# Performance work log

Hardware: AMD Instinct MI355X
Metric: run time of the kernel (lower is better)

Reference implementation:

```python
import jax, jax.numpy as jnp
import numpy as np

D_MODEL = 1024
N_HEADS = 16
D_HEAD = D_MODEL // N_HEADS
SPARSE_THRESH = 0.09
MASK_FILL = -1e9


def setup_inputs() -> dict:
    key = jax.random.key(0)
    ks = jax.random.split(key, 11)
    B, S, D = 4, 1024, D_MODEL
    # Xavier-uniform bound for square [D, D] linear weights
    bound = float(np.sqrt(6.0 / (D + D)))

    def xavier(k):
        return jax.random.uniform(k, (D, D), jnp.float32, -bound, bound)

    return {
        "q": jax.random.normal(ks[0], (B, S, D), jnp.float32),
        "k": jax.random.normal(ks[1], (B, S, D), jnp.float32),
        "v": jax.random.normal(ks[2], (B, S, D), jnp.float32),
        "Wq": xavier(ks[3]), "bq": jnp.zeros((D,), jnp.float32),
        "Wk": xavier(ks[4]), "bk": jnp.zeros((D,), jnp.float32),
        "Wv": xavier(ks[5]), "bv": jnp.zeros((D,), jnp.float32),
        "Wo": xavier(ks[6]), "bo": jnp.zeros((D,), jnp.float32),
    }


def reference(q, k, v, Wq, bq, Wk, bk, Wv, bv, Wo, bo):
    B, S, D = q.shape
    H, dk = N_HEADS, D_HEAD

    def proj(x, W, b):
        # nn.Linear: x @ W^T + b, then split heads -> [B, H, S, dk]
        y = jnp.einsum("bsd,ed->bse", x, W) + b
        return y.reshape(B, S, H, dk).transpose(0, 2, 1, 3)

    qh = proj(q, Wq, bq)
    kh = proj(k, Wk, bk)
    vh = proj(v, Wv, bv)

    scale = 1.0 / jnp.sqrt(jnp.asarray(dk, q.dtype))
    scores = jnp.einsum("bhqd,bhkd->bhqk", qh, kh) * scale  # [B,H,S,S]

    att1 = jax.nn.softmax(scores, axis=-1)
    # mask entries whose first-pass probability is below the sparsity threshold
    scores2 = jnp.where(att1 < SPARSE_THRESH, jnp.asarray(MASK_FILL, scores.dtype), scores)
    att2 = jax.nn.softmax(scores2, axis=-1)
    # dropout(p=0.2) is identity in eval mode (deterministic reference)

    ctx = jnp.einsum("bhqk,bhkd->bhqd", att2, vh)           # [B,H,S,dk]
    ctx = ctx.transpose(0, 2, 1, 3).reshape(B, S, D)
    return jnp.einsum("bsd,ed->bse", ctx, Wo) + bo
```

## Files before the change

### kernel.cpp

```cpp
#include <hip/hip_runtime.h>
#include <hip/hip_bf16.h>
#include <math.h>


constexpr int D_MODEL = 1024;
constexpr int N_HEADS = 16;
constexpr int D_HEAD  = 64;
constexpr int SEQ     = 1024;
constexpr int BATCH   = 4;
constexpr float SPARSE_THRESH = 0.09f;

typedef short  bf16x8 __attribute__((ext_vector_type(8)));
typedef float  f32x4  __attribute__((ext_vector_type(4)));

__device__ __forceinline__ unsigned short f2bf_rne(float x) {
    unsigned u = __float_as_uint(x);
    u += 0x7FFFu + ((u >> 16) & 1u);
    return (unsigned short)(u >> 16);
}
__device__ __forceinline__ float bf2f(unsigned short b) {
    return __uint_as_float(((unsigned)b) << 16);
}

__device__ __forceinline__ unsigned cvt2(float a, float b) {
    __hip_bfloat162 p = __float22bfloat162_rn(make_float2(a, b));
    unsigned u; __builtin_memcpy(&u, &p, 4); return u;
}
__device__ __forceinline__ void split4(float x0, float x1, float x2, float x3,
                                       unsigned* hw, unsigned* lw) {
    const unsigned uh0 = cvt2(x0, x1);
    hw[0] = uh0;
    lw[0] = cvt2(x0 - __uint_as_float(uh0 << 16),
                 x1 - __uint_as_float(uh0 & 0xFFFF0000u));
    const unsigned uh1 = cvt2(x2, x3);
    hw[1] = uh1;
    lw[1] = cvt2(x2 - __uint_as_float(uh1 << 16),
                 x3 - __uint_as_float(uh1 & 0xFFFF0000u));
}

union BF8 { unsigned u[4]; bf16x8 v; };

__device__ __forceinline__ void unpack_pair(const unsigned* u, bf16x8& hi, bf16x8& lo) {
    BF8 h, l;
    #pragma unroll
    for (int p = 0; p < 4; ++p) {
        h.u[p] = (u[2 * p] >> 16)      | (u[2 * p + 1] & 0xFFFF0000u);
        l.u[p] = (u[2 * p] & 0xFFFFu)  | (u[2 * p + 1] << 16);
    }
    hi = h.v; lo = l.v;
}

__device__ __forceinline__ void gld_lds16(const void* g, void* l) {
    __builtin_amdgcn_global_load_lds(
        (const __attribute__((address_space(1))) void*)g,
        (__attribute__((address_space(3))) void*)l, 16, 0, 0);
}

__global__ __launch_bounds__(256)
void conv_w(const float* __restrict__ Wq, const float* __restrict__ Wk,
            const float* __restrict__ Wv,
            unsigned short* __restrict__ Wqh, unsigned short* __restrict__ Wql,
            unsigned short* __restrict__ Wkh, unsigned short* __restrict__ Wkl,
            unsigned short* __restrict__ Wvh, unsigned short* __restrict__ Wvl)
{
    const int NW8 = (D_MODEL * D_MODEL) / 8;
    int i = blockIdx.x * 256 + threadIdx.x;
    const float* s; unsigned short *dh, *dl;
    if (i < NW8)            { s = Wq; dh = Wqh; dl = Wql; }
    else if (i < 2 * NW8)   { i -= NW8; s = Wk; dh = Wkh; dl = Wkl; }
    else                    { i -= 2 * NW8; s = Wv; dh = Wvh; dl = Wvl; }
    const float4 x0 = ((const float4*)(s + (size_t)i * 8))[0];
    const float4 x1 = ((const float4*)(s + (size_t)i * 8))[1];
    unsigned hw[4], lw[4];
    split4(x0.x, x0.y, x0.z, x0.w, &hw[0], &lw[0]);
    split4(x1.x, x1.y, x1.z, x1.w, &hw[2], &lw[2]);
    *(uint4*)&dh[(size_t)i * 8] = *(const uint4*)hw;
    *(uint4*)&dl[(size_t)i * 8] = *(const uint4*)lw;
}

__global__ __launch_bounds__(256, 3)
void proj_qkv(const float* __restrict__ q, const float* __restrict__ k,
              const float* __restrict__ v,
              const unsigned short* __restrict__ Wqh, const unsigned short* __restrict__ Wql,
              const unsigned short* __restrict__ Wkh, const unsigned short* __restrict__ Wkl,
              const unsigned short* __restrict__ Wvh, const unsigned short* __restrict__ Wvl,
              const float* __restrict__ bq, const float* __restrict__ bk,
              const float* __restrict__ bv,
              unsigned* __restrict__ qp,
              unsigned short* __restrict__ khh, unsigned short* __restrict__ khl,
              unsigned short* __restrict__ vt)
{
    __shared__ unsigned short SM[4][128][40];
    unsigned short (*A_h)[40] = SM[0];
    unsigned short (*A_l)[40] = SM[1];
    unsigned short (*B_h)[40] = SM[2];
    unsigned short (*B_l)[40] = SM[3];

    const int z = blockIdx.z;
    const float* X    = (z == 0) ? q   : (z == 1) ? k   : v;
    const unsigned short* Wh = (z == 0) ? Wqh : (z == 1) ? Wkh : Wvh;
    const unsigned short* Wl = (z == 0) ? Wql : (z == 1) ? Wkl : Wvl;
    const float* bias = (z == 0) ? bq  : (z == 1) ? bk  : bv;

    const int K = D_MODEL;
    const int tid = threadIdx.x, lane = tid & 63;
    const int l15 = lane & 15, l4 = lane >> 4;
    const int wv4 = tid >> 6;
    const int wr = (wv4 >> 1) * 64, wc = (wv4 & 1) * 64;
    const int bm = blockIdx.x * 128, bn = blockIdx.y * 128;
    const int sr = tid >> 1, sh = (tid & 1) * 16;

    f32x4 acc[4][4];
    #pragma unroll
    for (int i = 0; i < 4; ++i)
        #pragma unroll
        for (int j = 0; j < 4; ++j) acc[i][j] = (f32x4){0.f, 0.f, 0.f, 0.f};

    const float* ga = X + (size_t)(bm + sr) * K + sh;
    const unsigned short* gbh = Wh + (size_t)(bn + sr) * K + sh;
    const unsigned short* gbl = Wl + (size_t)(bn + sr) * K + sh;

    float4 av[4];
    uint4 wbh0, wbh1, wbl0, wbl1;
    #pragma unroll
    for (int l = 0; l < 4; ++l) av[l] = *(const float4*)&ga[l * 4];
    wbh0 = *(const uint4*)&gbh[0]; wbh1 = *(const uint4*)&gbh[8];
    wbl0 = *(const uint4*)&gbl[0]; wbl1 = *(const uint4*)&gbl[8];

    #pragma unroll 1
    for (int k0 = 0; k0 < K; k0 += 32) {
        unsigned ahw[8], alw[8];
        #pragma unroll
        for (int l = 0; l < 4; ++l)
            split4(av[l].x, av[l].y, av[l].z, av[l].w, &ahw[l * 2], &alw[l * 2]);

        __syncthreads();
        *(uint4*)&A_h[sr][sh]     = *(const uint4*)&ahw[0];
        *(uint4*)&A_h[sr][sh + 8] = *(const uint4*)&ahw[4];
        *(uint4*)&A_l[sr][sh]     = *(const uint4*)&alw[0];
        *(uint4*)&A_l[sr][sh + 8] = *(const uint4*)&alw[4];
        *(uint4*)&B_h[sr][sh]     = wbh0;
        *(uint4*)&B_h[sr][sh + 8] = wbh1;
        *(uint4*)&B_l[sr][sh]     = wbl0;
        *(uint4*)&B_l[sr][sh + 8] = wbl1;
        __syncthreads();

        if (k0 + 32 < K) {
            const int o = k0 + 32;
            #pragma unroll
            for (int l = 0; l < 4; ++l) av[l] = *(const float4*)&ga[o + l * 4];
            wbh0 = *(const uint4*)&gbh[o]; wbh1 = *(const uint4*)&gbh[o + 8];
            wbl0 = *(const uint4*)&gbl[o]; wbl1 = *(const uint4*)&gbl[o + 8];
        }

        bf16x8 ah[4], al4[4], bh4[4], bl4[4];
        #pragma unroll
        for (int i = 0; i < 4; ++i) {
            const int r = wr + i * 16 + l15;
            const int c = wc + i * 16 + l15;
            ah[i]  = *(const bf16x8*)&A_h[r][l4 * 8];
            al4[i] = *(const bf16x8*)&A_l[r][l4 * 8];
            bh4[i] = *(const bf16x8*)&B_h[c][l4 * 8];
            bl4[i] = *(const bf16x8*)&B_l[c][l4 * 8];
        }
        #pragma unroll
        for (int i = 0; i < 4; ++i)
            #pragma unroll
            for (int j = 0; j < 4; ++j) {
                acc[i][j] = __builtin_amdgcn_mfma_f32_16x16x32_bf16(ah[i],  bh4[j], acc[i][j], 0, 0, 0);
                acc[i][j] = __builtin_amdgcn_mfma_f32_16x16x32_bf16(ah[i],  bl4[j], acc[i][j], 0, 0, 0);
                acc[i][j] = __builtin_amdgcn_mfma_f32_16x16x32_bf16(al4[i], bh4[j], acc[i][j], 0, 0, 0);
            }
    }

    if (z == 2) {
        unsigned short* T = &SM[0][0][0];
        __syncthreads();
        #pragma unroll
        for (int i = 0; i < 4; ++i)
            #pragma unroll
            for (int j = 0; j < 4; ++j) {
                const int cl = wc + j * 16 + l15;
                const int sl = wr + i * 16 + l4 * 4;
                const float bi = bias[bn + cl];
                unsigned short h4[4];
                #pragma unroll
                for (int r = 0; r < 4; ++r)
                    h4[r] = f2bf_rne(acc[i][j][r] + bi);
                *(uint2*)&T[cl * 136 + sl] = *(const uint2*)&h4[0];
            }
        __syncthreads();
        const int c = tid >> 1, half = tid & 1;
        const int bb = bm >> 10;
        const int sb = (bm & (SEQ - 1)) + half * 64;
        unsigned short* dst = vt + (((size_t)bb << 20) + (size_t)(bn + c) * SEQ + sb);
        const unsigned short* srcT = &T[c * 136 + half * 64];
        #pragma unroll
        for (int u = 0; u < 8; ++u)
            *(uint4*)&dst[u * 8] = *(const uint4*)&srcT[u * 8];
        return;
    }

    if (z == 0) {
        #pragma unroll
        for (int i = 0; i < 4; ++i)
            #pragma unroll
            for (int j = 0; j < 4; ++j) {
                const int rb = bm + wr + i * 16 + l4 * 4;
                const int c  = bn + wc + j * 16 + l15;
                const float bi = bias[c];
                const int h = c >> 6, d = c & (D_HEAD - 1);
                #pragma unroll
                for (int r = 0; r < 4; ++r) {
                    const float val = (acc[i][j][r] + bi) * 0.125f;
                    const unsigned short hu = f2bf_rne(val);
                    const unsigned short lu = f2bf_rne(val - bf2f(hu));
                    const int mrow = rb + r;
                    const int b = mrow >> 10, s = mrow & (SEQ - 1);
                    qp[((size_t)(b * N_HEADS + h) * SEQ + s) * D_HEAD + d] =
                        ((unsigned)hu << 16) | lu;
                }
            }
    } else {
        #pragma unroll
        for (int i = 0; i < 4; ++i)
            #pragma unroll
            for (int j = 0; j < 4; ++j) {
                const int rb = bm + wr + i * 16 + l4 * 4;
                const int c  = bn + wc + j * 16 + l15;
                const float bi = bias[c];
                const int h = c >> 6, d = c & (D_HEAD - 1);
                #pragma unroll
                for (int r = 0; r < 4; ++r) {
                    const float val = acc[i][j][r] + bi;
                    const unsigned short hu = f2bf_rne(val);
                    const unsigned short lu = f2bf_rne(val - bf2f(hu));
                    const int mrow = rb + r;
                    const int b = mrow >> 10, s = mrow & (SEQ - 1);
                    const int dsw = d ^ ((s & 7) << 3);
                    const size_t off = ((size_t)(b * N_HEADS + h) * SEQ + s) * D_HEAD + dsw;
                    khh[off] = hu;
                    khl[off] = lu;
                }
            }
    }
}

__global__ __launch_bounds__(256, 3)
void proj_o(const unsigned short* __restrict__ Act, const float* __restrict__ W,
            const float* __restrict__ bias, float* __restrict__ out)
{
    __shared__ unsigned short A_h[128][40];
    __shared__ unsigned short B_h[128][40];

    const int K = D_MODEL;
    const int tid = threadIdx.x, lane = tid & 63;
    const int l15 = lane & 15, l4 = lane >> 4;
    const int wv4 = tid >> 6;
    const int wr = (wv4 >> 1) * 64, wc = (wv4 & 1) * 64;
    const int bm = blockIdx.x * 128, bn = blockIdx.y * 128;
    const int sr = tid >> 1, sh = (tid & 1) * 16;

    f32x4 acc[4][4];
    #pragma unroll
    for (int i = 0; i < 4; ++i)
        #pragma unroll
        for (int j = 0; j < 4; ++j) acc[i][j] = (f32x4){0.f, 0.f, 0.f, 0.f};

    const unsigned short* ga = Act + (size_t)(bm + sr) * K + sh;
    const float* gb = W + (size_t)(bn + sr) * K + sh;

    uint4 av0 = *(const uint4*)&ga[0], av1 = *(const uint4*)&ga[8];
    float4 bv4[4];
    #pragma unroll
    for (int l = 0; l < 4; ++l) bv4[l] = *(const float4*)&gb[l * 4];

    #pragma unroll 1
    for (int k0 = 0; k0 < K; k0 += 32) {
        unsigned bhw[8];
        #pragma unroll
        for (int l = 0; l < 4; ++l) {
            bhw[l * 2]     = cvt2(bv4[l].x, bv4[l].y);
            bhw[l * 2 + 1] = cvt2(bv4[l].z, bv4[l].w);
        }

        __syncthreads();
        *(uint4*)&A_h[sr][sh]     = av0;
        *(uint4*)&A_h[sr][sh + 8] = av1;
        *(uint4*)&B_h[sr][sh]     = *(const uint4*)&bhw[0];
        *(uint4*)&B_h[sr][sh + 8] = *(const uint4*)&bhw[4];
        __syncthreads();

        if (k0 + 32 < K) {
            av0 = *(const uint4*)&ga[k0 + 32];
            av1 = *(const uint4*)&ga[k0 + 32 + 8];
            #pragma unroll
            for (int l = 0; l < 4; ++l)
                bv4[l] = *(const float4*)&gb[k0 + 32 + l * 4];
        }

        bf16x8 ah[4], bh4[4];
        #pragma unroll
        for (int i = 0; i < 4; ++i) {
            ah[i]  = *(const bf16x8*)&A_h[wr + i * 16 + l15][l4 * 8];
            bh4[i] = *(const bf16x8*)&B_h[wc + i * 16 + l15][l4 * 8];
        }
        #pragma unroll
        for (int i = 0; i < 4; ++i)
            #pragma unroll
            for (int j = 0; j < 4; ++j)
                acc[i][j] = __builtin_amdgcn_mfma_f32_16x16x32_bf16(ah[i], bh4[j], acc[i][j], 0, 0, 0);
    }

    #pragma unroll
    for (int i = 0; i < 4; ++i)
        #pragma unroll
        for (int j = 0; j < 4; ++j) {
            const int rb = bm + wr + i * 16 + l4 * 4;
            const int c  = bn + wc + j * 16 + l15;
            const float bi = bias[c];
            #pragma unroll
            for (int r = 0; r < 4; ++r)
                out[(size_t)(rb + r) * D_MODEL + c] = acc[i][j][r] + bi;
        }
}

__device__ __forceinline__ void score_from_lds(
    const unsigned short (* __restrict__ KH)[64], const unsigned short (* __restrict__ KL)[64],
    int l15, int dk0, int dk1,
    const bf16x8 (&qh)[2][2], const bf16x8 (&ql)[2][2], f32x4 acc[2][4])
{
    #pragma unroll
    for (int j = 0; j < 4; ++j) {
        const int row = l15 + 16 * j;
        const bf16x8 kh0 = *(const bf16x8*)&KH[row][dk0];
        const bf16x8 kh1 = *(const bf16x8*)&KH[row][dk1];
        const bf16x8 kl0 = *(const bf16x8*)&KL[row][dk0];
        const bf16x8 kl1 = *(const bf16x8*)&KL[row][dk1];
        #pragma unroll
        for (int st = 0; st < 2; ++st) {
            f32x4 a = (f32x4){0.f, 0.f, 0.f, 0.f};
            a = __builtin_amdgcn_mfma_f32_16x16x32_bf16(qh[st][0], kh0, a, 0, 0, 0);
            a = __builtin_amdgcn_mfma_f32_16x16x32_bf16(qh[st][0], kl0, a, 0, 0, 0);
            a = __builtin_amdgcn_mfma_f32_16x16x32_bf16(ql[st][0], kh0, a, 0, 0, 0);
            a = __builtin_amdgcn_mfma_f32_16x16x32_bf16(qh[st][1], kh1, a, 0, 0, 0);
            a = __builtin_amdgcn_mfma_f32_16x16x32_bf16(qh[st][1], kl1, a, 0, 0, 0);
            a = __builtin_amdgcn_mfma_f32_16x16x32_bf16(ql[st][1], kh1, a, 0, 0, 0);
            acc[st][j] = a;
        }
    }
}

__global__ __launch_bounds__(256, 3)
void attn_mfma(const unsigned* __restrict__ qp,
               const unsigned short* __restrict__ khh, const unsigned short* __restrict__ khl,
               const unsigned short* __restrict__ vt, unsigned short* __restrict__ ctxh)
{
    __shared__ unsigned short KHL[2][2][64][64];
    __shared__ unsigned short Wl[4][32][64];
    __shared__ float Vm[64];
    __shared__ int AnyNU;
    float (*Pm)[4] = (float (*)[4])&Wl[0][0][0];

    const int tid  = threadIdx.x;
    const int lane = tid & 63;
    const int wv   = tid >> 6;
    const int l15  = lane & 15, l4 = lane >> 4;
    const int bh   = blockIdx.x;
    const int b    = bh >> 4, h = bh & 15;
    const int q0   = blockIdx.y * 128 + wv * 32;

    const int swz = (l15 & 7) << 3;
    const int dk0 = (l4 * 8) ^ swz;
    const int dk1 = (32 + l4 * 8) ^ swz;

    bf16x8 qh[2][2], ql[2][2];
    #pragma unroll
    for (int st = 0; st < 2; ++st) {
        const unsigned* qrow = qp + ((size_t)bh * SEQ + q0 + st * 16 + l15) * D_HEAD;
        #pragma unroll
        for (int ks = 0; ks < 2; ++ks) {
            unsigned u[8];
            *(uint4*)&u[0] = *(const uint4*)&qrow[ks * 32 + l4 * 8];
            *(uint4*)&u[4] = *(const uint4*)&qrow[ks * 32 + l4 * 8 + 4];
            unpack_pair(u, qh[st][ks], ql[st][ks]);
        }
    }

    const unsigned short* vtb = vt + (size_t)bh * D_HEAD * SEQ;

    {
        const int d = tid >> 2, q4 = tid & 3;
        const unsigned short* vr = vtb + (size_t)d * SEQ + q4 * 256;
        float s0 = 0.f, s1 = 0.f, s2 = 0.f, s3 = 0.f;
        #pragma unroll 4
        for (int i = 0; i < 32; ++i) {
            bf16x8 v8 = *(const bf16x8*)&vr[i * 8];
            s0 += bf2f((unsigned short)v8[0]) + bf2f((unsigned short)v8[4]);
            s1 += bf2f((unsigned short)v8[1]) + bf2f((unsigned short)v8[5]);
            s2 += bf2f((unsigned short)v8[2]) + bf2f((unsigned short)v8[6]);
            s3 += bf2f((unsigned short)v8[3]) + bf2f((unsigned short)v8[7]);
        }
        Pm[d][q4] = (s0 + s1) + (s2 + s3);
        if (tid == 0) AnyNU = 0;
    }

    const size_t kbase = (size_t)bh * SEQ * D_HEAD;
    const int krow0 = wv * 16 + (lane >> 3);
    const int dgrp  = (lane & 7) * 8;

    #pragma unroll
    for (int t = 0; t < 2; ++t) {
        const size_t src = kbase + (size_t)(krow0 + t * 8) * D_HEAD + dgrp;
        gld_lds16(khh + src, &KHL[0][0][wv * 16 + t * 8][0]);
        gld_lds16(khl + src, &KHL[0][1][wv * 16 + t * 8][0]);
    }
    __syncthreads();

    if (tid < 64)
        Vm[tid] = (Pm[tid][0] + Pm[tid][1] + Pm[tid][2] + Pm[tid][3]) * (1.f / 1024.f);

    float mloc[2][4], zloc[2][4];
    #pragma unroll
    for (int st = 0; st < 2; ++st)
        #pragma unroll
        for (int r = 0; r < 4; ++r) { mloc[st][r] = -1e30f; zloc[st][r] = 0.f; }

    int cur = 0;

    #pragma unroll 1
    for (int c = 0; c < 16; ++c) {
        const int cn = (c + 1) & 15;
        const int nxt = cur ^ 1;
        #pragma unroll
        for (int t = 0; t < 2; ++t) {
            const size_t src = kbase + ((size_t)cn * 64 + krow0 + t * 8) * D_HEAD + dgrp;
            gld_lds16(khh + src, &KHL[nxt][0][wv * 16 + t * 8][0]);
            gld_lds16(khl + src, &KHL[nxt][1][wv * 16 + t * 8][0]);
        }

        f32x4 acc[2][4];
        score_from_lds(KHL[cur][0], KHL[cur][1], l15, dk0, dk1, qh, ql, acc);

        #pragma unroll
        for (int st = 0; st < 2; ++st)
            #pragma unroll
            for (int r = 0; r < 4; ++r) {
                const float a0 = acc[st][0][r], a1 = acc[st][1][r];
                const float a2 = acc[st][2][r], a3 = acc[st][3][r];
                mloc[st][r] = fmaxf(mloc[st][r], fmaxf(fmaxf(a0, a1), fmaxf(a2, a3)));
                zloc[st][r] += (__expf(a0) + __expf(a1)) + (__expf(a2) + __expf(a3));
            }

        __syncthreads();
        cur = nxt;
    }

    float taue[2][4];
    bool  unif[2][4];
    int mynu = 0;
    #pragma unroll
    for (int st = 0; st < 2; ++st)
        #pragma unroll
        for (int r = 0; r < 4; ++r) {
            float mm = mloc[st][r], zz = zloc[st][r];
            #pragma unroll
            for (int o = 1; o <= 8; o <<= 1) {
                mm = fmaxf(mm, __shfl_xor(mm, o, 16));
                zz += __shfl_xor(zz, o, 16);
            }
            const float tau = __logf(SPARSE_THRESH * zz);
            const bool uni = (mm < tau);
            unif[st][r] = uni;
            taue[st][r] = uni ? 3.0e38f : tau;
            mynu |= uni ? 0 : 1;
        }
    if (__any(mynu)) { if (lane == 0) atomicOr(&AnyNU, 1); }
    __syncthreads();
    const bool runB = (AnyNU != 0);

    float z2[2][4];
    f32x4 pv[2][4];
    #pragma unroll
    for (int st = 0; st < 2; ++st)
        #pragma unroll
        for (int r = 0; r < 4; ++r) { z2[st][r] = 0.f; pv[st][r] = (f32x4){0.f, 0.f, 0.f, 0.f}; }

    if (runB) {
        #pragma unroll 1
        for (int c = 0; c < 16; ++c) {
            const int cn = (c + 1) & 15;
            const int nxt = cur ^ 1;
            #pragma unroll
            for (int t = 0; t < 2; ++t) {
                const size_t src = kbase + ((size_t)cn * 64 + krow0 + t * 8) * D_HEAD + dgrp;
                gld_lds16(khh + src, &KHL[nxt][0][wv * 16 + t * 8][0]);
                gld_lds16(khl + src, &KHL[nxt][1][wv * 16 + t * 8][0]);
            }

            f32x4 acc[2][4];
            score_from_lds(KHL[cur][0], KHL[cur][1], l15, dk0, dk1, qh, ql, acc);

            int any = 0;
            #pragma unroll
            for (int st = 0; st < 2; ++st)
                #pragma unroll
                for (int r = 0; r < 4; ++r) {
                    const float rmax = fmaxf(fmaxf(acc[st][0][r], acc[st][1][r]),
                                             fmaxf(acc[st][2][r], acc[st][3][r]));
                    any |= (rmax >= taue[st][r]) ? 1 : 0;
                }

            if (__any(any)) {
                #pragma unroll
                for (int st = 0; st < 2; ++st)
                    #pragma unroll
                    for (int j = 0; j < 4; ++j)
                        #pragma unroll
                        for (int r = 0; r < 4; ++r) {
                            const float a = acc[st][j][r];
                            const float w = (a >= taue[st][r]) ? __expf(a) : 0.f;
                            const unsigned short wb = f2bf_rne(w);
                            z2[st][r] += bf2f(wb);
                            Wl[wv][st * 16 + l4 * 4 + r][l15 + 16 * j] = wb;
                        }
                asm volatile("s_waitcnt lgkmcnt(0)" ::: "memory");
                __builtin_amdgcn_sched_barrier(0);

                bf16x8 wa[2][2];
                #pragma unroll
                for (int st = 0; st < 2; ++st)
                    #pragma unroll
                    for (int ks = 0; ks < 2; ++ks)
                        wa[st][ks] = *(const bf16x8*)&Wl[wv][st * 16 + l15][ks * 32 + l4 * 8];

                #pragma unroll
                for (int ds = 0; ds < 4; ++ds) {
                    const bf16x8 v0 = *(const bf16x8*)
                        &vtb[(size_t)(ds * 16 + l15) * SEQ + c * 64 + l4 * 8];
                    const bf16x8 v1 = *(const bf16x8*)
                        &vtb[(size_t)(ds * 16 + l15) * SEQ + c * 64 + 32 + l4 * 8];
                    #pragma unroll
                    for (int st = 0; st < 2; ++st) {
                        pv[st][ds] = __builtin_amdgcn_mfma_f32_16x16x32_bf16(wa[st][0], v0, pv[st][ds], 0, 0, 0);
                        pv[st][ds] = __builtin_amdgcn_mfma_f32_16x16x32_bf16(wa[st][1], v1, pv[st][ds], 0, 0, 0);
                    }
                }
            }

            __syncthreads();
            cur = nxt;
        }

        #pragma unroll
        for (int st = 0; st < 2; ++st)
            #pragma unroll
            for (int r = 0; r < 4; ++r) {
                #pragma unroll
                for (int o = 1; o <= 8; o <<= 1) z2[st][r] += __shfl_xor(z2[st][r], o, 16);
            }
    }

    float* Tw = (float*)&KHL[0][0][0][0] + wv * 2048;
    __syncthreads();
    #pragma unroll
    for (int st = 0; st < 2; ++st)
        #pragma unroll
        for (int r = 0; r < 4; ++r) {
            const float inv = unif[st][r] ? 0.f : (1.f / z2[st][r]);
            const int row = st * 16 + l4 * 4 + r;
            #pragma unroll
            for (int ds = 0; ds < 4; ++ds) {
                const int d = ds * 16 + l15;
                Tw[row * 64 + d] = unif[st][r] ? Vm[d] : pv[st][ds][r] * inv;
            }
        }
    asm volatile("s_waitcnt lgkmcnt(0)" ::: "memory");
    __builtin_amdgcn_sched_barrier(0);

    const int rr = lane >> 1, seg = lane & 1;
    const size_t gbase = ((size_t)b * SEQ + q0 + rr) * D_MODEL + h * D_HEAD + seg * 32;
    #pragma unroll
    for (int u2 = 0; u2 < 8; ++u2) {
        const float4 t = *(const float4*)&Tw[rr * 64 + seg * 32 + u2 * 4];
        unsigned short h4[4] = {f2bf_rne(t.x), f2bf_rne(t.y), f2bf_rne(t.z), f2bf_rne(t.w)};
        *(uint2*)&ctxh[gbase + u2 * 4] = *(const uint2*)h4;
    }
}

extern "C" void kernel_launch(void* const* d_in, const int* in_sizes, int n_in,
                              void* d_out, int out_size, void* d_ws, size_t ws_size,
                              hipStream_t stream)
{
    const float* q  = (const float*)d_in[0];
    const float* k  = (const float*)d_in[1];
    const float* v  = (const float*)d_in[2];
    const float* Wq = (const float*)d_in[3];
    const float* bq = (const float*)d_in[4];
    const float* Wk = (const float*)d_in[5];
    const float* bk = (const float*)d_in[6];
    const float* Wv = (const float*)d_in[7];
    const float* bv = (const float*)d_in[8];
    const float* Wo = (const float*)d_in[9];
    const float* bo = (const float*)d_in[10];
    float* out = (float*)d_out;

    const size_t MB = 1 << 20;
    char* w = (char*)d_ws;
    unsigned* qp = (unsigned*)(w);
    unsigned short* khh  = (unsigned short*)(w + 16 * MB);
    unsigned short* khl  = (unsigned short*)(w + 24 * MB);
    unsigned short* vt   = (unsigned short*)(w + 32 * MB);
    unsigned short* ctxh = (unsigned short*)(w + 40 * MB);
    unsigned short* Wqh = (unsigned short*)(w + 48 * MB);
    unsigned short* Wql = (unsigned short*)(w + 50 * MB);
    unsigned short* Wkh = (unsigned short*)(w + 52 * MB);
    unsigned short* Wkl = (unsigned short*)(w + 54 * MB);
    unsigned short* Wvh = (unsigned short*)(w + 56 * MB);
    unsigned short* Wvl = (unsigned short*)(w + 58 * MB);

    const int NW8 = (D_MODEL * D_MODEL) / 8;

    conv_w<<<(3 * NW8) / 256, 256, 0, stream>>>(Wq, Wk, Wv, Wqh, Wql, Wkh, Wkl, Wvh, Wvl);

    proj_qkv<<<dim3(32, 8, 3), 256, 0, stream>>>(q, k, v,
                                                 Wqh, Wql, Wkh, Wkl, Wvh, Wvl,
                                                 bq, bk, bv, qp, khh, khl, vt);

    attn_mfma<<<dim3(BATCH * N_HEADS, SEQ / 128), 256, 0, stream>>>(qp, khh, khl, vt, ctxh);

    proj_o<<<dim3(32, 8), 256, 0, stream>>>(ctxh, Wo, bo, out);
}
```

Before: 179.2 us.

## Triple-buffer K tiles in attention pass A with partial vmcnt waits

```diff
diff --git a/kernel.cpp b/kernel.cpp
--- a/kernel.cpp
+++ b/kernel.cpp
@@ -351,12 +351,12 @@
     }
 }
 
-__global__ __launch_bounds__(256, 3)
+__global__ __launch_bounds__(256, 2)
 void attn_mfma(const unsigned* __restrict__ qp,
                const unsigned short* __restrict__ khh, const unsigned short* __restrict__ khl,
                const unsigned short* __restrict__ vt, unsigned short* __restrict__ ctxh)
 {
-    __shared__ unsigned short KHL[2][2][64][64];
+    __shared__ unsigned short KHL[3][2][64][64];
     __shared__ unsigned short Wl[4][32][64];
     __shared__ float Vm[64];
     __shared__ int AnyNU;
@@ -409,12 +409,17 @@
     const int krow0 = wv * 16 + (lane >> 3);
     const int dgrp  = (lane & 7) * 8;
 
-    #pragma unroll
-    for (int t = 0; t < 2; ++t) {
-        const size_t src = kbase + (size_t)(krow0 + t * 8) * D_HEAD + dgrp;
-        gld_lds16(khh + src, &KHL[0][0][wv * 16 + t * 8][0]);
-        gld_lds16(khl + src, &KHL[0][1][wv * 16 + t * 8][0]);
-    }
+    #define STAGE_CHUNK(cidx, bufi)                                               \
+        {   const int _c = (cidx);                                                \
+            _Pragma("unroll")                                                     \
+            for (int t = 0; t < 2; ++t) {                                         \
+                const size_t src = kbase + ((size_t)_c * 64 + krow0 + t * 8) * D_HEAD + dgrp; \
+                gld_lds16(khh + src, &KHL[bufi][0][wv * 16 + t * 8][0]);          \
+                gld_lds16(khl + src, &KHL[bufi][1][wv * 16 + t * 8][0]);          \
+            } }
+
+    STAGE_CHUNK(0, 0);
+    STAGE_CHUNK(1, 1);
     __syncthreads();
 
     if (tid < 64)
@@ -426,21 +431,14 @@
         #pragma unroll
         for (int r = 0; r < 4; ++r) { mloc[st][r] = -1e30f; zloc[st][r] = 0.f; }
 
-    int cur = 0;
-
     #pragma unroll 1
     for (int c = 0; c < 16; ++c) {
-        const int cn = (c + 1) & 15;
-        const int nxt = cur ^ 1;
-        #pragma unroll
-        for (int t = 0; t < 2; ++t) {
-            const size_t src = kbase + ((size_t)cn * 64 + krow0 + t * 8) * D_HEAD + dgrp;
-            gld_lds16(khh + src, &KHL[nxt][0][wv * 16 + t * 8][0]);
-            gld_lds16(khl + src, &KHL[nxt][1][wv * 16 + t * 8][0]);
-        }
+        const int rb = c % 3;
+        const int ib = (c + 2) % 3;
+        STAGE_CHUNK((c + 2) & 15, ib);
 
         f32x4 acc[2][4];
-        score_from_lds(KHL[cur][0], KHL[cur][1], l15, dk0, dk1, qh, ql, acc);
+        score_from_lds(KHL[rb][0], KHL[rb][1], l15, dk0, dk1, qh, ql, acc);
 
         #pragma unroll
         for (int st = 0; st < 2; ++st)
@@ -452,8 +450,10 @@
                 zloc[st][r] += (__expf(a0) + __expf(a1)) + (__expf(a2) + __expf(a3));
             }
 
-        __syncthreads();
-        cur = nxt;
+        asm volatile("s_waitcnt vmcnt(4)" ::: "memory");
+        __builtin_amdgcn_sched_barrier(0);
+        __builtin_amdgcn_s_barrier();
+        __builtin_amdgcn_sched_barrier(0);
     }
 
     float taue[2][4];
@@ -487,19 +487,17 @@
         for (int r = 0; r < 4; ++r) { z2[st][r] = 0.f; pv[st][r] = (f32x4){0.f, 0.f, 0.f, 0.f}; }
 
     if (runB) {
+        STAGE_CHUNK(0, 0);
+        __syncthreads();
+
         #pragma unroll 1
         for (int c = 0; c < 16; ++c) {
-            const int cn = (c + 1) & 15;
-            const int nxt = cur ^ 1;
-            #pragma unroll
-            for (int t = 0; t < 2; ++t) {
-                const size_t src = kbase + ((size_t)cn * 64 + krow0 + t * 8) * D_HEAD + dgrp;
-                gld_lds16(khh + src, &KHL[nxt][0][wv * 16 + t * 8][0]);
-                gld_lds16(khl + src, &KHL[nxt][1][wv * 16 + t * 8][0]);
-            }
+            const int rb = c % 3;
+            const int ib = (c + 1) % 3;
+            STAGE_CHUNK((c + 1) & 15, ib);
 
             f32x4 acc[2][4];
-            score_from_lds(KHL[cur][0], KHL[cur][1], l15, dk0, dk1, qh, ql, acc);
+            score_from_lds(KHL[rb][0], KHL[rb][1], l15, dk0, dk1, qh, ql, acc);
 
             int any = 0;
             #pragma unroll
@@ -549,7 +547,6 @@
             }
 
             __syncthreads();
-            cur = nxt;
         }
 
         #pragma unroll
@@ -586,6 +583,7 @@
         unsigned short h4[4] = {f2bf_rne(t.x), f2bf_rne(t.y), f2bf_rne(t.z), f2bf_rne(t.w)};
         *(uint2*)&ctxh[gbase + u2 * 4] = *(const uint2*)h4;
     }
+    #undef STAGE_CHUNK
 }
 
 extern "C" void kernel_launch(void* const* d_in, const int* in_sizes, int n_in,
```

New measurement: 183.2 us. 2.2% more time.
